# Kernel tuning notes

Hardware: AMD Instinct MI355X
Metric: run time of the kernel (lower is better)

Reference implementation:

```python
import jax, jax.numpy as jnp
import numpy as np

# Scalar quantization params (QLinear __init__ args)
FEATURE_BITWIDTH = 8
WEIGHT_BITWIDTH = 8
INPUT_ZERO_POINT = -3
OUTPUT_ZERO_POINT = -5
INPUT_SCALE = 0.05
OUTPUT_SCALE = 0.1
QMIN = -(1 << (FEATURE_BITWIDTH - 1))   # -128
QMAX = (1 << (FEATURE_BITWIDTH - 1)) - 1  # 127

M, K, N = 8192, 4096, 4096


def float_to_fixed_point(x, bitwidth):
    """Represent x (0 < x < 1) as int_scale * 2^-frac_bits with int_scale
    in [2^(bitwidth-2), 2^(bitwidth-1)) (mantissa fits in signed `bitwidth` bits)."""
    frac_bits = (bitwidth - 1 - jnp.ceil(jnp.log2(x))).astype(jnp.int32)
    int_scale = jnp.round(x * jnp.exp2(frac_bits.astype(jnp.float32))).astype(jnp.int32)
    return int_scale, frac_bits


def setup_inputs() -> dict:
    key = jax.random.key(0)
    k1, k2, k3, k4 = jax.random.split(key, 4)
    qinput = jax.random.randint(k1, (M, K), -128, 128, dtype=jnp.int8)
    qweight = jax.random.randint(k2, (N, K), -128, 128, dtype=jnp.int8)
    qbias = jax.random.randint(k3, (N,), -(1 << 16), 1 << 16, dtype=jnp.int32)
    # per-output-channel weight scale; keeps folded scale in (0, 1)
    weight_scale = jax.random.uniform(k4, (N,), jnp.float32, 0.002, 0.02)
    return {"qinput": qinput, "qweight": qweight, "qbias": qbias,
            "weight_scale": weight_scale}


def reference(qinput, qweight, qbias, weight_scale):
    w32 = qweight.astype(jnp.int32)                      # [N, K]
    # Qbias' = qbias - sum_k(qweight) * Zin  (bias shift folding input zero point)
    shifted_qbias = qbias - w32.sum(axis=1) * INPUT_ZERO_POINT  # [N]
    # int32 GEMM: [M, K] @ [K, N] + bias
    acc = qinput.astype(jnp.int32) @ w32.T + shifted_qbias[None, :]  # [M, N]
    # fixed-point requantization: (acc * int_scale) >> frac_bits + Zout
    folded_scale = INPUT_SCALE * weight_scale / OUTPUT_SCALE         # [N], in (0,1)
    int_scale, frac_bits = float_to_fixed_point(folded_scale, FEATURE_BITWIDTH)
    # widen to int64 for the multiply so the (acc * int_scale) product cannot wrap
    prod = acc.astype(jnp.int64) * int_scale.astype(jnp.int64)[None, :]
    scaled = jnp.right_shift(prod, frac_bits.astype(jnp.int64)[None, :])  # arithmetic >>
    out = scaled + OUTPUT_ZERO_POINT
    return jnp.clip(out, QMIN, QMAX).astype(jnp.int8)
```

## Files before the change

kernel.cpp:

```cpp
#include <hip/hip_runtime.h>
#include <cstdint>
#include <cstddef>

#define M_DIM 8192
#define N_DIM 4096
#define K_DIM 4096

#define BM 128
#define BN 128
#define BK 128

#define BM2 256
#define BN2 256
#define BK2 128
#define NKT (K_DIM / BK2)

typedef int int32x4  __attribute__((ext_vector_type(4)));
typedef int int32x16 __attribute__((ext_vector_type(16)));


typedef __attribute__((address_space(1))) const void* gas_cptr;
typedef __attribute__((address_space(3))) void* las_ptr;

__device__ __forceinline__ void async_copy16(const void* g, void* l) {
    __builtin_amdgcn_global_load_lds((gas_cptr)g, (las_ptr)l, 16, 0, 0);
}

__device__ __forceinline__ int32x4 pack16(const int* p) {
    const int32x4* v = (const int32x4*)p;
    int32x4 w0 = v[0], w1 = v[1], w2 = v[2], w3 = v[3];
    int32x4 r;
    r.x = (w0.x & 0xFF) | ((w0.y & 0xFF) << 8) | ((w0.z & 0xFF) << 16) | (w0.w << 24);
    r.y = (w1.x & 0xFF) | ((w1.y & 0xFF) << 8) | ((w1.z & 0xFF) << 16) | (w1.w << 24);
    r.z = (w2.x & 0xFF) | ((w2.y & 0xFF) << 8) | ((w2.z & 0xFF) << 16) | (w2.w << 24);
    r.w = (w3.x & 0xFF) | ((w3.y & 0xFF) << 8) | ((w3.z & 0xFF) << 16) | (w3.w << 24);
    return r;
}

__global__ void ql_detect_kernel(const int* a, const int* b, int* ws) {
    int t = threadIdx.x;
    int fa = 0, fb = 0;
    for (int i = t; i < 4096; i += 64) {
        int va = a[i]; if (va > 127 || va < -128) fa = 1;
        int vb = b[i]; if (vb > 127 || vb < -128) fb = 1;
    }
    unsigned long long ba = __ballot(fa);
    unsigned long long bb = __ballot(fb);
    if (t == 0) { ws[0] = ba ? 1 : 0; ws[1] = bb ? 1 : 0; }
}

__global__ __launch_bounds__(256)
void ql_pack2_kernel(const void* wsrc, int* wdst, const void* asrc, int* adst,
                     const int* ws, long ndwW, long ndwA) {
    const int fA = __builtin_amdgcn_readfirstlane(ws[0]);
    const int fW = __builtin_amdgcn_readfirstlane(ws[1]);
    const long nW = fW ? 0 : ndwW;
    const long nA = fA ? 0 : ndwA;
    const long total = nW + nA;
    const long stride = (long)gridDim.x * 256;
    for (long c = (long)blockIdx.x * 256 + threadIdx.x; c < total; c += stride) {
        if (c < nW) {
            int32x4 v = ((const int32x4*)wsrc)[c];
            wdst[c] = (v.x & 0xFF) | ((v.y & 0xFF) << 8) | ((v.z & 0xFF) << 16) | (v.w << 24);
        } else {
            const long ca = c - nW;
            int32x4 v = ((const int32x4*)asrc)[ca];
            adst[ca] = (v.x & 0xFF) | ((v.y & 0xFF) << 8) | ((v.z & 0xFF) << 16) | (v.w << 24);
        }
    }
}

__global__ void ql_prep8_kernel(const void* worig, const int8_t* w8p, const int* qbias,
                                const float* wscale, int* ws) {
    const int fb = __builtin_amdgcn_readfirstlane(ws[1]);
    const int8_t* w8 = fb ? (const int8_t*)worig : w8p;

    const int lane = threadIdx.x & 63;
    const int wid  = threadIdx.x >> 6;
    const int n = blockIdx.x * 4 + wid;

    const int32x4* row = (const int32x4*)(w8 + (size_t)n * K_DIM);
    int s = 0;
    for (int c = lane; c < K_DIM / 16; c += 64) {
        int32x4 v = row[c];
#pragma unroll
        for (int j = 0; j < 4; ++j) {
            int w = (j == 0) ? v.x : (j == 1) ? v.y : (j == 2) ? v.z : v.w;
            s += (int)(int8_t)(w) + (int)(int8_t)(w >> 8)
               + (int)(int8_t)(w >> 16) + (w >> 24);
        }
    }
#pragma unroll
    for (int off = 32; off > 0; off >>= 1) s += __shfl_down(s, off, 64);

    if (lane == 0) {
        ws[16 + n] = qbias[n] + 3 * s;
        float folded = (0.05f * wscale[n]) / 0.1f;
        int fbits = (int)(7.0f - ceilf(log2f(folded)));
        int isc = (int)rintf(folded * exp2f((float)fbits));
        ws[16 + N_DIM + n] = isc;
        ws[16 + 2 * N_DIM + n] = fbits;
    }
}

__global__ void ql_prep_kernel(const void* wptr, const int* qbias,
                               const float* wscale, int* ws) {
    const int lane = threadIdx.x & 63;
    const int wid  = threadIdx.x >> 6;
    const int n = blockIdx.x * 4 + wid;
    const int b8 = __builtin_amdgcn_readfirstlane(ws[1]);

    int s = 0;
    if (b8) {
        const int32x4* row = (const int32x4*)((const int8_t*)wptr + (size_t)n * K_DIM);
        for (int c = lane; c < K_DIM / 16; c += 64) {
            int32x4 v = row[c];
#pragma unroll
            for (int j = 0; j < 4; ++j) {
                int w = (j == 0) ? v.x : (j == 1) ? v.y : (j == 2) ? v.z : v.w;
                s += (int)(int8_t)(w) + (int)(int8_t)(w >> 8)
                   + (int)(int8_t)(w >> 16) + (w >> 24);
            }
        }
    } else {
        const int32x4* row = (const int32x4*)((const int*)wptr + (size_t)n * K_DIM);
        for (int c = lane; c < K_DIM / 4; c += 64) {
            int32x4 v = row[c];
            s += v.x + v.y + v.z + v.w;
        }
    }
#pragma unroll
    for (int off = 32; off > 0; off >>= 1) s += __shfl_down(s, off, 64);

    if (lane == 0) {
        ws[16 + n] = qbias[n] + 3 * s;
        float folded = (0.05f * wscale[n]) / 0.1f;
        int fbits = (int)(7.0f - ceilf(log2f(folded)));
        int isc = (int)rintf(folded * exp2f((float)fbits));
        ws[16 + N_DIM + n] = isc;
        ws[16 + 2 * N_DIM + n] = fbits;
    }
}

__device__ __forceinline__ void ql_epilogue(int32x4 acc[4][4], const int* ws,
                                            int* out, int bm, int bn,
                                            int wm, int wn, int qm, int qh) {
    const int* qb  = ws + 16;
    const int* isc = ws + 16 + N_DIM;
    const int* fbt = ws + 16 + 2 * N_DIM;
#pragma unroll
    for (int j = 0; j < 4; ++j) {
        const int n_g = bn * BN + wn + j * 16 + qm;
        const int b0 = qb[n_g];
        const int s0 = isc[n_g];
        const int f0 = fbt[n_g];
#pragma unroll
        for (int i = 0; i < 4; ++i) {
            const int m_base = bm * BM + wm + i * 16 + qh * 4;
#pragma unroll
            for (int r = 0; r < 4; ++r) {
                int v = ((r == 0) ? acc[i][j].x : (r == 1) ? acc[i][j].y
                        : (r == 2) ? acc[i][j].z : acc[i][j].w) + b0;
                long long p = (long long)v * (long long)s0;
                int o = (int)(p >> f0) - 5;
                o = o < -128 ? -128 : (o > 127 ? 127 : o);
                out[(size_t)(m_base + r) * N_DIM + n_g] = o;
            }
        }
    }
}


#define TILE2(BUF, TT) do { \
    _Pragma("unroll") for (int ml = 0; ml < 2; ++ml) \
    _Pragma("unroll") for (int kc = 0; kc < 4; ++kc) \
        afL[ml][kc] = LA[BUF][baseAe[kc] + ml * 256]; \
    _Pragma("unroll") for (int kc = 0; kc < 4; ++kc) \
        bf0[kc] = LB[BUF][baseBe[kc]]; \
    _Pragma("unroll") for (int kc = 0; kc < 4; ++kc) \
        bf1[kc] = LB[BUF][baseBe[kc] + 256]; \
    _Pragma("unroll") for (int ml = 0; ml < 2; ++ml) \
    _Pragma("unroll") for (int kc = 0; kc < 4; ++kc) \
        afH[ml][kc] = LA[BUF][baseAe[kc] + 512 + ml * 256]; \
    if ((TT) + 1 < NKT) { \
        _Pragma("unroll") for (int h2 = 0; h2 < 4; ++h2) { \
            async_copy16(gA + (size_t)((TT) + 1) * 128 + (size_t)h2 * 262144, \
                         &LA[(BUF) ^ 1][h2 * 512 + t]); \
            async_copy16(gB + (size_t)((TT) + 1) * 128 + (size_t)h2 * 262144, \
                         &LB[(BUF) ^ 1][h2 * 512 + t]); \
        } \
    } \
    __builtin_amdgcn_s_setprio(1); \
    _Pragma("unroll") for (int kc = 0; kc < 4; ++kc) \
    _Pragma("unroll") for (int ml = 0; ml < 2; ++ml) \
        acc[ml][0] = __builtin_amdgcn_mfma_i32_32x32x32_i8(afL[ml][kc], bf0[kc], acc[ml][0], 0, 0, 0); \
    _Pragma("unroll") for (int kc = 0; kc < 4; ++kc) \
    _Pragma("unroll") for (int ml = 0; ml < 2; ++ml) \
        acc[ml][1] = __builtin_amdgcn_mfma_i32_32x32x32_i8(afL[ml][kc], bf1[kc], acc[ml][1], 0, 0, 0); \
    _Pragma("unroll") for (int kc = 0; kc < 4; ++kc) \
    _Pragma("unroll") for (int ml = 0; ml < 2; ++ml) \
        acc[2 + ml][0] = __builtin_amdgcn_mfma_i32_32x32x32_i8(afH[ml][kc], bf0[kc], acc[2 + ml][0], 0, 0, 0); \
    _Pragma("unroll") for (int kc = 0; kc < 4; ++kc) \
    _Pragma("unroll") for (int ml = 0; ml < 2; ++ml) \
        acc[2 + ml][1] = __builtin_amdgcn_mfma_i32_32x32x32_i8(afH[ml][kc], bf1[kc], acc[2 + ml][1], 0, 0, 0); \
    __builtin_amdgcn_s_setprio(0); \
    __syncthreads(); \
} while (0)

__global__ __launch_bounds__(512, 2)
void ql_gemm8_kernel(const void* a0, const int8_t* a8,
                     const void* b0, const int8_t* w8,
                     const int* ws, int* out) {
    __shared__ int32x4 LA[2][2048];
    __shared__ int32x4 LB[2][2048];

    const int fa = __builtin_amdgcn_readfirstlane(ws[0]);
    const int fb = __builtin_amdgcn_readfirstlane(ws[1]);
    const int8_t* aptr = fa ? (const int8_t*)a0 : a8;
    const int8_t* bptr = fb ? (const int8_t*)b0 : w8;

    const int t    = threadIdx.x;
    const int lane = t & 63;
    const int wid  = t >> 6;
    const int wr   = wid >> 2;
    const int wc   = wid & 3;
    const int l31  = lane & 31;
    const int hi   = lane >> 5;

    const int bn = blockIdx.x;
    const int bm = blockIdx.y;
    const int arow0 = bm * BM2;
    const int brow0 = bn * BN2;

    const int fr = (lane & 7) ^ ((l31 >> 3) & 3);
    int baseAe[4], baseBe[4];
#pragma unroll
    for (int kc = 0; kc < 4; ++kc) {
        const int phys = (kc * 2 + hi) ^ fr;
        baseAe[kc] = (wr * 128 + l31) * 8 + phys;
        baseBe[kc] = (wc * 64  + l31) * 8 + phys;
    }

    const int colg = (t & 7) ^ ((t >> 3) & 7) ^ ((t >> 6) & 3);
    const int8_t* gA = aptr + (size_t)(arow0 + (t >> 3)) * K_DIM + colg * 16;
    const int8_t* gB = bptr + (size_t)(brow0 + (t >> 3)) * K_DIM + colg * 16;

    int32x16 acc[4][2] = {};
    int32x4 afL[2][4], afH[2][4], bf0[4], bf1[4];

#pragma unroll
    for (int h2 = 0; h2 < 4; ++h2) {
        async_copy16(gA + (size_t)h2 * 262144, &LA[0][h2 * 512 + t]);
        async_copy16(gB + (size_t)h2 * 262144, &LB[0][h2 * 512 + t]);
    }
    __syncthreads();

#pragma unroll 1
    for (int T = 0; T < NKT; T += 2) {
        TILE2(0, T);
        TILE2(1, T + 1);
    }

    const int* qb  = ws + 16;
    const int* isc = ws + 16 + N_DIM;
    const int* fbt = ws + 16 + 2 * N_DIM;
#pragma unroll
    for (int j = 0; j < 2; ++j) {
        const int n_g = bn * BN2 + wc * 64 + j * 32 + l31;
        const int b0r = qb[n_g];
        const int s0r = isc[n_g];
        const int f0r = fbt[n_g];
#pragma unroll
        for (int i = 0; i < 4; ++i) {
            const int m0 = bm * BM2 + wr * 128 + i * 32 + hi * 4;
#pragma unroll
            for (int reg = 0; reg < 16; ++reg) {
                const int row = (reg & 3) + 8 * (reg >> 2);
                int v = acc[i][j][reg] + b0r;
                long long p = (long long)v * (long long)s0r;
                int o = (int)(p >> f0r) - 5;
                o = o < -128 ? -128 : (o > 127 ? 127 : o);
                out[(size_t)(m0 + row) * N_DIM + n_g] = o;
            }
        }
    }
}

__global__ __launch_bounds__(256)
void ql_gemm_fb_kernel(const void* aptr, const void* bptr, const int* ws, int* out) {
    __shared__ int32x4 Als[BM * BK / 16];
    __shared__ int32x4 Bls[BN * BK / 16];

    const int a8 = __builtin_amdgcn_readfirstlane(ws[0]);
    const int b8 = __builtin_amdgcn_readfirstlane(ws[1]);

    const int t    = threadIdx.x;
    const int lane = t & 63;
    const int wid  = t >> 6;
    const int bn = blockIdx.x;
    const int bm = blockIdx.y;

    const int wm = (wid >> 1) * 64;
    const int wn = (wid & 1) * 64;
    const int qm = lane & 15;
    const int qh = lane >> 4;

    int32x4 acc[4][4] = {};

    for (int kt = 0; kt < K_DIM / BK; ++kt) {
        __syncthreads();
        const int k0 = kt * BK;
#pragma unroll
        for (int r = 0; r < 4; ++r) {
            const int c    = r * 256 + t;
            const int row  = c >> 3;
            const int colg = (c & 7) ^ (row & 7);
            const size_t offA = (size_t)(bm * BM + row) * K_DIM + k0 + colg * 16;
            const size_t offB = (size_t)(bn * BN + row) * K_DIM + k0 + colg * 16;
            if (a8) async_copy16((const int8_t*)aptr + offA, &Als[c]);
            else    Als[c] = pack16((const int*)aptr + offA);
            if (b8) async_copy16((const int8_t*)bptr + offB, &Bls[c]);
            else    Bls[c] = pack16((const int*)bptr + offB);
        }
        __syncthreads();

#pragma unroll
        for (int s = 0; s < 2; ++s) {
            const int colk = s * 4 + qh;
            int32x4 af[4], bf[4];
#pragma unroll
            for (int i = 0; i < 4; ++i) {
                const int ra = wm + i * 16 + qm;
                const int rb = wn + i * 16 + qm;
                af[i] = Als[ra * 8 + (colk ^ (ra & 7))];
                bf[i] = Bls[rb * 8 + (colk ^ (rb & 7))];
            }
#pragma unroll
            for (int i = 0; i < 4; ++i)
#pragma unroll
                for (int j = 0; j < 4; ++j)
                    acc[i][j] = __builtin_amdgcn_mfma_i32_16x16x64_i8(
                        af[i], bf[j], acc[i][j], 0, 0, 0);
        }
    }
    ql_epilogue(acc, ws, out, bm, bn, wm, wn, qm, qh);
}

extern "C" void kernel_launch(void* const* d_in, const int* in_sizes, int n_in,
                              void* d_out, int out_size, void* d_ws, size_t ws_size,
                              hipStream_t stream) {
    const void* qin    = d_in[0];
    const void* qwt    = d_in[1];
    const int* qbias   = (const int*)d_in[2];
    const float* wscal = (const float*)d_in[3];
    int* ws  = (int*)d_ws;
    int* out = (int*)d_out;

    hipLaunchKernelGGL(ql_detect_kernel, dim3(1), dim3(64), 0, stream,
                       (const int*)qin, (const int*)qwt, ws);

    const size_t need = 65536 + (size_t)M_DIM * K_DIM + (size_t)N_DIM * K_DIM;
    if (ws_size >= need) {
        int8_t* a8 = (int8_t*)d_ws + 65536;
        int8_t* w8 = a8 + (size_t)M_DIM * K_DIM;
        const long ndwA = (long)M_DIM * K_DIM / 4;
        const long ndwW = (long)N_DIM * K_DIM / 4;
        const long ndwT = ndwA + ndwW;
        hipLaunchKernelGGL(ql_pack2_kernel, dim3((unsigned)(ndwT / (256 * 4))), dim3(256),
                           0, stream, qwt, (int*)w8, qin, (int*)a8, ws, ndwW, ndwA);
        hipLaunchKernelGGL(ql_prep8_kernel, dim3(N_DIM / 4), dim3(256), 0, stream,
                           qwt, w8, qbias, wscal, ws);
        hipLaunchKernelGGL(ql_gemm8_kernel, dim3(N_DIM / BN2, M_DIM / BM2), dim3(512),
                           0, stream, qin, a8, qwt, w8, ws, out);
    } else {
        hipLaunchKernelGGL(ql_prep_kernel, dim3(N_DIM / 4), dim3(256), 0, stream,
                           qwt, qbias, wscal, ws);
        hipLaunchKernelGGL(ql_gemm_fb_kernel, dim3(N_DIM / BN, M_DIM / BM), dim3(256), 0, stream,
                           qin, qwt, ws, out);
    }
}
```

Measured before the change: 414.4 us.

## Split K-tile into half phases with vmcnt waits, XCD-aware block swizzle, nontemporal IO

The int8 GEMM main loop is restructured so each 128-wide K tile is processed in two 64-wide half phases. Each phase waits with an explicit vmcnt and raw barrier instead of a full __syncthreads, which spreads global-to-LDS copies more finely across the MFMA work. The LDS layout and swizzle change to 64-byte rows to match. Block indices are remapped so neighbouring tiles land on the same XCD for better L2 reuse, and the pack loads and output stores become nontemporal. The finer barriers and the hand-set vmcnt counts add risk of races or LDS bank conflicts.

```diff
diff --git a/kernel.cpp b/kernel.cpp
--- a/kernel.cpp
+++ b/kernel.cpp
@@ -51,22 +51,23 @@
 
 __global__ __launch_bounds__(256)
 void ql_pack2_kernel(const void* wsrc, int* wdst, const void* asrc, int* adst,
-                     const int* ws, long ndwW, long ndwA) {
+                     const int* ws) {
     const int fA = __builtin_amdgcn_readfirstlane(ws[0]);
     const int fW = __builtin_amdgcn_readfirstlane(ws[1]);
+    const long ndwW = (long)N_DIM * K_DIM / 4;
+    const long ndwA = (long)M_DIM * K_DIM / 4;
     const long nW = fW ? 0 : ndwW;
     const long nA = fA ? 0 : ndwA;
     const long total = nW + nA;
     const long stride = (long)gridDim.x * 256;
     for (long c = (long)blockIdx.x * 256 + threadIdx.x; c < total; c += stride) {
-        if (c < nW) {
-            int32x4 v = ((const int32x4*)wsrc)[c];
-            wdst[c] = (v.x & 0xFF) | ((v.y & 0xFF) << 8) | ((v.z & 0xFF) << 16) | (v.w << 24);
-        } else {
-            const long ca = c - nW;
-            int32x4 v = ((const int32x4*)asrc)[ca];
-            adst[ca] = (v.x & 0xFF) | ((v.y & 0xFF) << 8) | ((v.z & 0xFF) << 16) | (v.w << 24);
-        }
+        const int32x4* src;
+        int* dst;
+        long i;
+        if (c < nW) { src = (const int32x4*)wsrc; dst = wdst; i = c; }
+        else        { src = (const int32x4*)asrc; dst = adst; i = c - nW; }
+        int32x4 v = __builtin_nontemporal_load(&src[i]);
+        dst[i] = (v.x & 0xFF) | ((v.y & 0xFF) << 8) | ((v.z & 0xFF) << 16) | (v.w << 24);
     }
 }
 
@@ -171,40 +172,33 @@
 }
 
 
-#define TILE2(BUF, TT) do { \
-    _Pragma("unroll") for (int ml = 0; ml < 2; ++ml) \
-    _Pragma("unroll") for (int kc = 0; kc < 4; ++kc) \
-        afL[ml][kc] = LA[BUF][baseAe[kc] + ml * 256]; \
-    _Pragma("unroll") for (int kc = 0; kc < 4; ++kc) \
-        bf0[kc] = LB[BUF][baseBe[kc]]; \
-    _Pragma("unroll") for (int kc = 0; kc < 4; ++kc) \
-        bf1[kc] = LB[BUF][baseBe[kc] + 256]; \
-    _Pragma("unroll") for (int ml = 0; ml < 2; ++ml) \
-    _Pragma("unroll") for (int kc = 0; kc < 4; ++kc) \
-        afH[ml][kc] = LA[BUF][baseAe[kc] + 512 + ml * 256]; \
-    if ((TT) + 1 < NKT) { \
-        _Pragma("unroll") for (int h2 = 0; h2 < 4; ++h2) { \
-            async_copy16(gA + (size_t)((TT) + 1) * 128 + (size_t)h2 * 262144, \
-                         &LA[(BUF) ^ 1][h2 * 512 + t]); \
-            async_copy16(gB + (size_t)((TT) + 1) * 128 + (size_t)h2 * 262144, \
-                         &LB[(BUF) ^ 1][h2 * 512 + t]); \
+#define PHASE(BUF, KH, TT, VMC, DOST) do { \
+    asm volatile("s_waitcnt vmcnt(" #VMC ")" ::: "memory"); \
+    __builtin_amdgcn_s_barrier(); \
+    _Pragma("unroll") for (int kr = 0; kr < 2; ++kr) { \
+        _Pragma("unroll") for (int ml = 0; ml < 2; ++ml) { \
+            aL[ml][kr] = LA[BUF][baseA[KH][kr] + ml * 128]; \
+            aH[ml][kr] = LA[BUF][baseA[KH][kr] + 256 + ml * 128]; \
         } \
+        b0f[kr] = LB[BUF][baseB[KH][kr]]; \
+        b1f[kr] = LB[BUF][baseB[KH][kr] + 128]; \
+    } \
+    if (DOST) { \
+        const size_t so = (size_t)((TT) + 1) * 128 + (KH) * 64; \
+        async_copy16(gA + so,          &LA[(BUF) ^ 1][(KH) * 1024 + t]); \
+        async_copy16(gA + so + 524288, &LA[(BUF) ^ 1][(KH) * 1024 + 512 + t]); \
+        async_copy16(gB + so,          &LB[(BUF) ^ 1][(KH) * 1024 + t]); \
+        async_copy16(gB + so + 524288, &LB[(BUF) ^ 1][(KH) * 1024 + 512 + t]); \
     } \
     __builtin_amdgcn_s_setprio(1); \
-    _Pragma("unroll") for (int kc = 0; kc < 4; ++kc) \
-    _Pragma("unroll") for (int ml = 0; ml < 2; ++ml) \
-        acc[ml][0] = __builtin_amdgcn_mfma_i32_32x32x32_i8(afL[ml][kc], bf0[kc], acc[ml][0], 0, 0, 0); \
-    _Pragma("unroll") for (int kc = 0; kc < 4; ++kc) \
-    _Pragma("unroll") for (int ml = 0; ml < 2; ++ml) \
-        acc[ml][1] = __builtin_amdgcn_mfma_i32_32x32x32_i8(afL[ml][kc], bf1[kc], acc[ml][1], 0, 0, 0); \
-    _Pragma("unroll") for (int kc = 0; kc < 4; ++kc) \
-    _Pragma("unroll") for (int ml = 0; ml < 2; ++ml) \
-        acc[2 + ml][0] = __builtin_amdgcn_mfma_i32_32x32x32_i8(afH[ml][kc], bf0[kc], acc[2 + ml][0], 0, 0, 0); \
-    _Pragma("unroll") for (int kc = 0; kc < 4; ++kc) \
-    _Pragma("unroll") for (int ml = 0; ml < 2; ++ml) \
-        acc[2 + ml][1] = __builtin_amdgcn_mfma_i32_32x32x32_i8(afH[ml][kc], bf1[kc], acc[2 + ml][1], 0, 0, 0); \
+    _Pragma("unroll") for (int kr = 0; kr < 2; ++kr) \
+    _Pragma("unroll") for (int ml = 0; ml < 2; ++ml) { \
+        acc[ml][0]     = __builtin_amdgcn_mfma_i32_32x32x32_i8(aL[ml][kr], b0f[kr], acc[ml][0], 0, 0, 0); \
+        acc[ml][1]     = __builtin_amdgcn_mfma_i32_32x32x32_i8(aL[ml][kr], b1f[kr], acc[ml][1], 0, 0, 0); \
+        acc[2 + ml][0] = __builtin_amdgcn_mfma_i32_32x32x32_i8(aH[ml][kr], b0f[kr], acc[2 + ml][0], 0, 0, 0); \
+        acc[2 + ml][1] = __builtin_amdgcn_mfma_i32_32x32x32_i8(aH[ml][kr], b1f[kr], acc[2 + ml][1], 0, 0, 0); \
+    } \
     __builtin_amdgcn_s_setprio(0); \
-    __syncthreads(); \
 } while (0)
 
 __global__ __launch_bounds__(512, 2)
@@ -227,39 +221,55 @@
     const int l31  = lane & 31;
     const int hi   = lane >> 5;
 
-    const int bn = blockIdx.x;
-    const int bm = blockIdx.y;
+    const int flat = blockIdx.y * gridDim.x + blockIdx.x;
+    const int xcd  = flat & 7;
+    const int lid  = flat >> 3;
+    const int g    = lid >> 5;
+    const int r    = lid & 31;
+    const int bm   = xcd * 4 + g * 2 + (r & 1);
+    const int bn   = r >> 1;
+
     const int arow0 = bm * BM2;
     const int brow0 = bn * BN2;
 
-    const int fr = (lane & 7) ^ ((l31 >> 3) & 3);
-    int baseAe[4], baseBe[4];
-#pragma unroll
-    for (int kc = 0; kc < 4; ++kc) {
-        const int phys = (kc * 2 + hi) ^ fr;
-        baseAe[kc] = (wr * 128 + l31) * 8 + phys;
-        baseBe[kc] = (wc * 64  + l31) * 8 + phys;
-    }
-
-    const int colg = (t & 7) ^ ((t >> 3) & 7) ^ ((t >> 6) & 3);
-    const int8_t* gA = aptr + (size_t)(arow0 + (t >> 3)) * K_DIM + colg * 16;
-    const int8_t* gB = bptr + (size_t)(brow0 + (t >> 3)) * K_DIM + colg * 16;
+    const int fr31 = (l31 >> 1) & 3;
+    int baseA[2][2], baseB[2][2];
+#pragma unroll
+    for (int kh = 0; kh < 2; ++kh)
+#pragma unroll
+        for (int kr = 0; kr < 2; ++kr) {
+            const int phys = (kr * 2 + hi) ^ fr31;
+            baseA[kh][kr] = kh * 1024 + (wr * 128 + l31) * 4 + phys;
+            baseB[kh][kr] = kh * 1024 + (wc * 64  + l31) * 4 + phys;
+        }
+
+    const int row0 = t >> 2;
+    const int c0   = (t & 3) ^ ((t >> 3) & 3);
+    const int8_t* gA = aptr + (size_t)(arow0 + row0) * K_DIM + c0 * 16;
+    const int8_t* gB = bptr + (size_t)(brow0 + row0) * K_DIM + c0 * 16;
 
     int32x16 acc[4][2] = {};
-    int32x4 afL[2][4], afH[2][4], bf0[4], bf1[4];
-
-#pragma unroll
-    for (int h2 = 0; h2 < 4; ++h2) {
-        async_copy16(gA + (size_t)h2 * 262144, &LA[0][h2 * 512 + t]);
-        async_copy16(gB + (size_t)h2 * 262144, &LB[0][h2 * 512 + t]);
-    }
-    __syncthreads();
+    int32x4 aL[2][2], aH[2][2], b0f[2], b1f[2];
+
+#pragma unroll
+    for (int kh = 0; kh < 2; ++kh) {
+        async_copy16(gA + kh * 64,          &LA[0][kh * 1024 + t]);
+        async_copy16(gA + kh * 64 + 524288, &LA[0][kh * 1024 + 512 + t]);
+        async_copy16(gB + kh * 64,          &LB[0][kh * 1024 + t]);
+        async_copy16(gB + kh * 64 + 524288, &LB[0][kh * 1024 + 512 + t]);
+    }
 
 #pragma unroll 1
-    for (int T = 0; T < NKT; T += 2) {
-        TILE2(0, T);
-        TILE2(1, T + 1);
-    }
+    for (int T = 0; T < NKT - 2; T += 2) {
+        PHASE(0, 0, T, 4, true);
+        PHASE(0, 1, T, 4, true);
+        PHASE(1, 0, T + 1, 4, true);
+        PHASE(1, 1, T + 1, 4, true);
+    }
+    PHASE(0, 0, NKT - 2, 4, true);
+    PHASE(0, 1, NKT - 2, 4, true);
+    PHASE(1, 0, NKT - 1, 4, false);
+    PHASE(1, 1, NKT - 1, 0, false);
 
     const int* qb  = ws + 16;
     const int* isc = ws + 16 + N_DIM;
@@ -280,7 +290,7 @@
                 long long p = (long long)v * (long long)s0r;
                 int o = (int)(p >> f0r) - 5;
                 o = o < -128 ? -128 : (o > 127 ? 127 : o);
-                out[(size_t)(m0 + row) * N_DIM + n_g] = o;
+                __builtin_nontemporal_store(o, &out[(size_t)(m0 + row) * N_DIM + n_g]);
             }
         }
     }
@@ -363,11 +373,9 @@
     if (ws_size >= need) {
         int8_t* a8 = (int8_t*)d_ws + 65536;
         int8_t* w8 = a8 + (size_t)M_DIM * K_DIM;
-        const long ndwA = (long)M_DIM * K_DIM / 4;
-        const long ndwW = (long)N_DIM * K_DIM / 4;
-        const long ndwT = ndwA + ndwW;
+        const long ndwT = (long)M_DIM * K_DIM / 4 + (long)N_DIM * K_DIM / 4;
         hipLaunchKernelGGL(ql_pack2_kernel, dim3((unsigned)(ndwT / (256 * 4))), dim3(256),
-                           0, stream, qwt, (int*)w8, qin, (int*)a8, ws, ndwW, ndwA);
+                           0, stream, qwt, (int*)w8, qin, (int*)a8, ws);
         hipLaunchKernelGGL(ql_prep8_kernel, dim3(N_DIM / 4), dim3(256), 0, stream,
                            qwt, w8, qbias, wscal, ws);
         hipLaunchKernelGGL(ql_gemm8_kernel, dim3(N_DIM / BN2, M_DIM / BM2), dim3(512),
```

New measurement: 413.3 us. Within noise of the previous version (-0.3%).
